# Kernel tuning notes

Measured on AMD Instinct MI355X. Metric: run time of the kernel, lower is better.

Reference implementation:

```python
import jax, jax.numpy as jnp
import numpy as np

B, CI, CO, H, W, E, R, K = 32, 128, 256, 64, 64, 8, 16, 3


def setup_inputs() -> dict:
    key = jax.random.key(0)
    ks = jax.random.split(key, 12)
    def n(k, shape, scale):
        return jax.random.normal(k, shape, dtype=jnp.float32) * scale
    return {
        "x": n(ks[0], (B, CI, H, W), 1.0),
        "experts": n(ks[1], (E, CO, CI, K, K), 0.1),
        # routing SE: C -> C/R -> C -> E (1x1 convs == dense on pooled vec)
        "rw1": n(ks[2], (CI // R, CI), 0.05), "rb1": jnp.zeros((CI // R,), jnp.float32),
        "rw2": n(ks[3], (CI, CI // R), 0.05), "rb2": jnp.zeros((CI,), jnp.float32),
        "rw3": n(ks[4], (E, CI), 0.05),      "rb3": jnp.zeros((E,), jnp.float32),
        # channel attention SE on output: CO -> CO/R -> CO
        "aw1": n(ks[5], (CO // R, CO), 0.05), "ab1": jnp.zeros((CO // R,), jnp.float32),
        "aw2": n(ks[6], (CO, CO // R), 0.05), "ab2": jnp.zeros((CO,), jnp.float32),
    }


def reference(x, experts, rw1, rb1, rw2, rb2, rw3, rb3, aw1, ab1, aw2, ab2):
    # --- routing: SE-style gate -> softmax over experts ---
    pooled = x.mean(axis=(2, 3))                       # [B, CI]
    h = jax.nn.relu(pooled @ rw1.T + rb1)              # [B, CI/R]
    s = jax.nn.sigmoid(h @ rw2.T + rb2)                # [B, CI]
    rweights = jax.nn.softmax(s @ rw3.T + rb3, axis=1) # [B, E]
    # --- per-sample expert kernel combination ---
    w = jnp.einsum('be,eoihw->boihw', rweights, experts)  # [B, CO, CI, K, K]
    # --- per-sample conv (== grouped conv with groups=B) via vmap ---
    def conv1(xi, wi):
        # xi: [CI,H,W], wi: [CO,CI,K,K]
        return jax.lax.conv_general_dilated(
            xi[None], wi, window_strides=(1, 1), padding=[(1, 1), (1, 1)],
            dimension_numbers=('NCHW', 'OIHW', 'NCHW'))[0]
    out = jax.vmap(conv1)(x, w)                        # [B, CO, H, W]
    # --- channel attention on output ---
    p = out.mean(axis=(2, 3))                          # [B, CO]
    ca = jax.nn.sigmoid(jax.nn.relu(p @ aw1.T + ab1) @ aw2.T + ab2)
    return out * ca[:, :, None, None]
```

## Files before the change

### kernel.cpp

```cpp
#include <hip/hip_runtime.h>
#include <hip/hip_bf16.h>


#define BB 32
#define CI_ 128
#define CO_ 256
#define HW_ 4096
#define KK 1152

typedef unsigned short u16;
typedef __attribute__((ext_vector_type(8))) __bf16 bf16x8;
typedef __attribute__((ext_vector_type(4))) float floatx4;

typedef const __attribute__((address_space(1))) void* gptr_t;
typedef __attribute__((address_space(3))) void* sptr_t;

__device__ __forceinline__ void gload_lds16(const void* g, void* s) {
  __builtin_amdgcn_global_load_lds((gptr_t)g, (sptr_t)s, 16, 0, 0);
}

__global__ __launch_bounds__(256) void k_stats2(const float* __restrict__ x,
                                                float* __restrict__ Sr,
                                                float* __restrict__ pooled,
                                                unsigned* __restrict__ zp) {
  int blk = blockIdx.x;
  int tid = threadIdx.x;
  if (blk == 0 && tid < 64) zp[tid] = 0u;
  int b = blk >> 7, ci = blk & 127;
  const float4* xp = (const float4*)(x + ((size_t)(b * CI_ + ci) << 12));
  float T = 0.f, r0 = 0.f, r63 = 0.f, c0 = 0.f, c63 = 0.f;
  __shared__ float corn[4];
  __shared__ float wsum[4][5];
#pragma unroll
  for (int j = 0; j < 4; j++) {
    int idx = j * 256 + tid;
    float4 v = xp[idx];
    float rs = v.x + v.y + v.z + v.w;
    T += rs;
    int x16 = idx & 15;
    if (idx < 16)    r0  += rs;
    if (idx >= 1008) r63 += rs;
    if (x16 == 0)  c0  += v.x;
    if (x16 == 15) c63 += v.w;
    if (idx == 0)    corn[0] = v.x;
    if (idx == 15)   corn[1] = v.w;
    if (idx == 1008) corn[2] = v.x;
    if (idx == 1023) corn[3] = v.w;
  }
  for (int off = 32; off; off >>= 1) {
    T   += __shfl_down(T, off);
    r0  += __shfl_down(r0, off);
    r63 += __shfl_down(r63, off);
    c0  += __shfl_down(c0, off);
    c63 += __shfl_down(c63, off);
  }
  int w = tid >> 6, lane = tid & 63;
  if (lane == 0) { wsum[w][0]=T; wsum[w][1]=r0; wsum[w][2]=r63; wsum[w][3]=c0; wsum[w][4]=c63; }
  __syncthreads();
  if (tid == 0) {
    T   = wsum[0][0]+wsum[1][0]+wsum[2][0]+wsum[3][0];
    r0  = wsum[0][1]+wsum[1][1]+wsum[2][1]+wsum[3][1];
    r63 = wsum[0][2]+wsum[1][2]+wsum[2][2]+wsum[3][2];
    c0  = wsum[0][3]+wsum[1][3]+wsum[2][3]+wsum[3][3];
    c63 = wsum[0][4]+wsum[1][4]+wsum[2][4]+wsum[3][4];
    pooled[b * CI_ + ci] = T * (1.0f / 4096.0f);
#pragma unroll
    for (int ky = 0; ky < 3; ky++) {
#pragma unroll
      for (int kx = 0; kx < 3; kx++) {
        int dy = ky - 1, dx = kx - 1;
        float s = T;
        if (dy == -1) s -= r63;
        if (dy ==  1) s -= r0;
        if (dx == -1) s -= c63;
        if (dx ==  1) s -= c0;
        if (dy != 0 && dx != 0) s += corn[(dy == -1 ? 2 : 0) + (dx == -1 ? 1 : 0)];
        Sr[(b * 9 + ky * 3 + kx) * CI_ + ci] = s * (1.0f / 4096.0f);
      }
    }
  }
}

__global__ __launch_bounds__(256) void k_xform(const float* __restrict__ x,
                                               u16* __restrict__ xt) {
  int blk = blockIdx.x;
  int b = blk >> 6, y = blk & 63;
  __shared__ u16 ts[64][132];
  int tid = threadIdx.x;
  const float* xb = x + ((size_t)b << 19) + (y << 6);
#pragma unroll
  for (int it = 0; it < 8; it++) {
    int idx = it * 256 + tid;
    int ci = idx >> 4, x4 = idx & 15;
    float4 v = *(const float4*)(xb + (size_t)ci * 4096 + x4 * 4);
    __hip_bfloat16 h0 = __float2bfloat16(v.x), h1 = __float2bfloat16(v.y);
    __hip_bfloat16 h2 = __float2bfloat16(v.z), h3 = __float2bfloat16(v.w);
    int xx = x4 << 2;
    ts[xx + 0][ci] = *(const u16*)&h0;
    ts[xx + 1][ci] = *(const u16*)&h1;
    ts[xx + 2][ci] = *(const u16*)&h2;
    ts[xx + 3][ci] = *(const u16*)&h3;
  }
  __syncthreads();
  uint2* ot = (uint2*)(xt + ((size_t)b * HW_ + y * 64) * CI_);
#pragma unroll
  for (int it = 0; it < 8; it++) {
    int o = it * 256 + tid;
    int pix = o >> 5, c4 = o & 31;
    ot[o] = *(const uint2*)&ts[pix][c4 * 4];
  }
}

__global__ __launch_bounds__(128) void k_route2(const float* __restrict__ pooled,
    const float* __restrict__ rw1, const float* __restrict__ rb1,
    const float* __restrict__ rw2, const float* __restrict__ rb2,
    const float* __restrict__ rw3, const float* __restrict__ rb3,
    float* __restrict__ r) {
  int b = blockIdx.x, tid = threadIdx.x;
  int o = tid >> 4, l = tid & 15;
  __shared__ float ps[128], hs[8], ss[128], lg[8];
  ps[tid] = pooled[b * 128 + tid];
  __syncthreads();
  {
    float a = 0.f;
#pragma unroll
    for (int j = 0; j < 8; j++) a += ps[l * 8 + j] * rw1[o * 128 + l * 8 + j];
    a += __shfl_xor(a, 1); a += __shfl_xor(a, 2);
    a += __shfl_xor(a, 4); a += __shfl_xor(a, 8);
    if (l == 0) hs[o] = fmaxf(a + rb1[o], 0.f);
  }
  __syncthreads();
  {
    float a = rb2[tid];
#pragma unroll
    for (int j = 0; j < 8; j++) a += hs[j] * rw2[tid * 8 + j];
    ss[tid] = 1.f / (1.f + expf(-a));
  }
  __syncthreads();
  {
    float a = 0.f;
#pragma unroll
    for (int j = 0; j < 8; j++) a += ss[l * 8 + j] * rw3[o * 128 + l * 8 + j];
    a += __shfl_xor(a, 1); a += __shfl_xor(a, 2);
    a += __shfl_xor(a, 4); a += __shfl_xor(a, 8);
    if (l == 0) lg[o] = a + rb3[o];
  }
  __syncthreads();
  if (tid == 0) {
    float m = lg[0];
    for (int e = 1; e < 8; e++) m = fmaxf(m, lg[e]);
    float s = 0.f, ex[8];
    for (int e = 0; e < 8; e++) { ex[e] = expf(lg[e] - m); s += ex[e]; }
    for (int e = 0; e < 8; e++) r[b * 8 + e] = ex[e] / s;
  }
}

__global__ __launch_bounds__(256) void k_combine2(const float* __restrict__ experts,
                                                  const float* __restrict__ r,
                                                  const float* __restrict__ Sr,
                                                  __hip_bfloat16* __restrict__ wr,
                                                  float* __restrict__ p) {
  int co = blockIdx.x & 255, g = blockIdx.x >> 8;
  int tid = threadIdx.x;
  __shared__ float els[8][1152];
  __shared__ float rsh[32][8];
  __shared__ float pw[4];
#pragma unroll
  for (int it = 0; it < 9; it++) {
    int f = it * 256 + tid;
    int e = f / 288, q = f - e * 288;
    float4 ev = *(const float4*)(experts + (size_t)e * 294912 + (size_t)co * 1152 + q * 4);
    *(float4*)&els[e][q * 4] = ev;
  }
  rsh[tid >> 3][tid & 7] = r[tid];
  __syncthreads();
  int s = tid >> 7, ci = tid & 127;
  for (int bb = 0; bb < 4; bb++) {
    int b = g * 8 + bb * 2 + s;
    float rv[8];
#pragma unroll
    for (int e = 0; e < 8; e++) rv[e] = rsh[b][e];
    float pacc = 0.f;
    __hip_bfloat16* wrow = wr + (size_t)(b * 256 + co) * KK;
    const float* sb = Sr + b * KK;
#pragma unroll
    for (int k = 0; k < 9; k++) {
      float v = 0.f;
#pragma unroll
      for (int e = 0; e < 8; e++) v += rv[e] * els[e][ci * 9 + k];
      wrow[k * 128 + ci] = __float2bfloat16(v);
      pacc += v * sb[k * 128 + ci];
    }
    for (int off = 32; off; off >>= 1) pacc += __shfl_down(pacc, off);
    if ((tid & 63) == 0) pw[tid >> 6] = pacc;
    __syncthreads();
    if (ci == 0) p[b * 256 + co] = pw[s * 2] + pw[s * 2 + 1];
    __syncthreads();
  }
}

__global__ __launch_bounds__(256) void k_catt2(const float* __restrict__ p,
    const float* __restrict__ aw1, const float* __restrict__ ab1,
    const float* __restrict__ aw2, const float* __restrict__ ab2,
    float* __restrict__ ca) {
  int b = blockIdx.x, tid = threadIdx.x;
  int o = tid >> 4, l = tid & 15;
  __shared__ float ps[256], ts[16];
  ps[tid] = p[b * 256 + tid];
  __syncthreads();
  {
    float a = 0.f;
#pragma unroll
    for (int j = 0; j < 16; j++) a += ps[l * 16 + j] * aw1[o * 256 + l * 16 + j];
    a += __shfl_xor(a, 1); a += __shfl_xor(a, 2);
    a += __shfl_xor(a, 4); a += __shfl_xor(a, 8);
    if (l == 0) ts[o] = fmaxf(a + ab1[o], 0.f);
  }
  __syncthreads();
  float a = ab2[tid];
#pragma unroll
  for (int j = 0; j < 16; j++) a += ts[j] * aw2[tid * 16 + j];
  ca[b * 256 + tid] = 1.f / (1.f + expf(-a));
}

__global__ __launch_bounds__(256) void k_conv(const u16* __restrict__ xt,
                                              const u16* __restrict__ wr,
                                              const float* __restrict__ ca,
                                              const u16* __restrict__ zp,
                                              float* __restrict__ out) {
  int id = blockIdx.x;
  int b = (id & 7) | (((id >> 9) & 3) << 3);
  int rem = (id >> 3) & 63;
  int coT = rem >> 5, rp = rem & 31;
  int y0 = rp * 2;
  int coBase = coT * 128;
  int tid = threadIdx.x;
  int w = tid >> 6, lane = tid & 63;
  int wm = w & 1, wn = w >> 1;
  int quad = lane >> 4, l15 = lane & 15;
  int cl8 = lane & 7, lr = lane >> 3;

  __shared__ __align__(16) u16 As[128 * 64];
  __shared__ __align__(16) u16 Bs[128 * 64];

  const u16* aP[4];
  int dstO[4], chB[4], ylocB[4], xlocB[4];
#pragma unroll
  for (int ri = 0; ri < 4; ri++) {
    int rr = ri * 32 + w * 8 + lr;
    int c = cl8 ^ (rr & 7);
    aP[ri] = wr + (size_t)(b * 256 + coBase + rr) * KK + c * 8;
    dstO[ri] = rr * 64 + cl8 * 8;
    chB[ri] = c;
    ylocB[ri] = rr >> 6;
    xlocB[ri] = rr & 63;
  }

  int aOff[4][2], bOff[4][2];
#pragma unroll
  for (int i = 0; i < 4; i++) {
    int m = wm * 64 + i * 16 + l15;
    int n = wn * 64 + i * 16 + l15;
#pragma unroll
    for (int h = 0; h < 2; h++) {
      aOff[i][h] = m * 64 + ((((h << 2) | quad) ^ (m & 7)) << 3);
      bOff[i][h] = n * 64 + ((((h << 2) | quad) ^ (n & 7)) << 3);
    }
  }

  floatx4 acc[4][4];
#pragma unroll
  for (int i = 0; i < 4; i++)
#pragma unroll
    for (int j = 0; j < 4; j++) acc[i][j] = floatx4{0.f, 0.f, 0.f, 0.f};

  for (int kidx = 0; kidx < 9; kidx++) {
    int ky = kidx / 3, kx = kidx - ky * 3;
    const u16* bP[4];
    int bStep[4];
#pragma unroll
    for (int ri = 0; ri < 4; ri++) {
      int ys = y0 + ylocB[ri] + ky - 1;
      int xs = xlocB[ri] + kx - 1;
      bool valid = ((unsigned)ys < 64u) && ((unsigned)xs < 64u);
      bP[ri] = valid ? (xt + ((size_t)(b * HW_ + ys * 64 + xs) << 7) + chB[ri] * 8)
                     : (zp + chB[ri] * 8);
      bStep[ri] = valid ? 64 : 0;
    }
#pragma unroll
    for (int cib = 0; cib < 2; cib++) {
      __syncthreads();
#pragma unroll
      for (int ri = 0; ri < 4; ri++)
        gload_lds16(aP[ri] + kidx * 128 + cib * 64, &As[dstO[ri]]);
#pragma unroll
      for (int ri = 0; ri < 4; ri++)
        gload_lds16(bP[ri] + cib * bStep[ri], &Bs[dstO[ri]]);
      __syncthreads();
#pragma unroll
      for (int h = 0; h < 2; h++) {
        bf16x8 af[4], bfv[4];
#pragma unroll
        for (int i = 0; i < 4; i++) af[i] = *(const bf16x8*)&As[aOff[i][h]];
#pragma unroll
        for (int j = 0; j < 4; j++) bfv[j] = *(const bf16x8*)&Bs[bOff[j][h]];
#pragma unroll
        for (int i = 0; i < 4; i++)
#pragma unroll
          for (int j = 0; j < 4; j++)
            acc[i][j] = __builtin_amdgcn_mfma_f32_16x16x32_bf16(af[i], bfv[j], acc[i][j], 0, 0, 0);
      }
    }
  }

  float cav[4][4];
#pragma unroll
  for (int i = 0; i < 4; i++)
#pragma unroll
    for (int ri = 0; ri < 4; ri++)
      cav[i][ri] = ca[b * 256 + coBase + wm * 64 + i * 16 + quad * 4 + ri];
#pragma unroll
  for (int i = 0; i < 4; i++) {
#pragma unroll
    for (int j = 0; j < 4; j++) {
      int n = wn * 64 + j * 16 + l15;
      int yy = y0 + (n >> 6), xx = n & 63;
#pragma unroll
      for (int ri = 0; ri < 4; ri++) {
        int co = coBase + wm * 64 + i * 16 + quad * 4 + ri;
        out[((size_t)(b * 256 + co) << 12) + (yy << 6) + xx] = acc[i][j][ri] * cav[i][ri];
      }
    }
  }
}

extern "C" void kernel_launch(void* const* d_in, const int* in_sizes, int n_in,
                              void* d_out, int out_size, void* d_ws, size_t ws_size,
                              hipStream_t stream) {
  const float* x       = (const float*)d_in[0];
  const float* experts = (const float*)d_in[1];
  const float* rw1 = (const float*)d_in[2];
  const float* rb1 = (const float*)d_in[3];
  const float* rw2 = (const float*)d_in[4];
  const float* rb2 = (const float*)d_in[5];
  const float* rw3 = (const float*)d_in[6];
  const float* rb3 = (const float*)d_in[7];
  const float* aw1 = (const float*)d_in[8];
  const float* ab1 = (const float*)d_in[9];
  const float* aw2 = (const float*)d_in[10];
  const float* ab2 = (const float*)d_in[11];

  char* ws = (char*)d_ws;
  u16*   xt     = (u16*)(ws + 0);
  __hip_bfloat16* wr = (__hip_bfloat16*)(ws + 33554432);
  float* Sr     = (float*)(ws + 52428800);
  float* pooled = (float*)(ws + 52576256);
  float* r      = (float*)(ws + 52592640);
  float* p      = (float*)(ws + 52593664);
  float* ca     = (float*)(ws + 52626432);
  u16*   zp     = (u16*)(ws + 52659200);

  k_stats2<<<4096, 256, 0, stream>>>(x, Sr, pooled, (unsigned*)zp);
  k_xform<<<2048, 256, 0, stream>>>(x, xt);
  k_route2<<<32, 128, 0, stream>>>(pooled, rw1, rb1, rw2, rb2, rw3, rb3, r);
  k_combine2<<<1024, 256, 0, stream>>>(experts, r, Sr, wr, p);
  k_catt2<<<32, 256, 0, stream>>>(p, aw1, ab1, aw2, ab2, ca);
  k_conv<<<2048, 256, 0, stream>>>(xt, (const u16*)wr, ca, zp, (float*)d_out);
}
```

Before: 311.4 us.

## Enlarge conv tile to 256x256 with double-buffered LDS prefetch

The conv kernel now uses 512-thread blocks, each computing all 256 output channels for four image rows (a 256x256 output tile), instead of 128x128 tiles. LDS is double-buffered, so the next K-slice's global-to-LDS loads are issued before the current slice's MFMAs, and the loop needs one barrier per step instead of two. This is meant to reuse each input tile across all output channels, cut redundant loads, and hide load latency. In exchange it uses 128 accumulator registers per thread and 128KB of LDS per block, and launches only 512 blocks, which may limit occupancy.

After: 321.1 us. 3.1% more time.

```diff
diff --git a/kernel.cpp b/kernel.cpp
--- a/kernel.cpp
+++ b/kernel.cpp
@@ -223,112 +223,128 @@
   ca[b * 256 + tid] = 1.f / (1.f + expf(-a));
 }
 
-__global__ __launch_bounds__(256) void k_conv(const u16* __restrict__ xt,
-                                              const u16* __restrict__ wr,
-                                              const float* __restrict__ ca,
-                                              const u16* __restrict__ zp,
-                                              float* __restrict__ out) {
+__global__ __launch_bounds__(512, 2) void k_conv2p(const u16* __restrict__ xt,
+                                                   const u16* __restrict__ wr,
+                                                   const float* __restrict__ ca,
+                                                   const u16* __restrict__ zp,
+                                                   float* __restrict__ out) {
+  __shared__ __align__(16) u16 As[2 * 16384];
+  __shared__ __align__(16) u16 Bs[2 * 16384];
+
   int id = blockIdx.x;
-  int b = (id & 7) | (((id >> 9) & 3) << 3);
-  int rem = (id >> 3) & 63;
-  int coT = rem >> 5, rp = rem & 31;
-  int y0 = rp * 2;
-  int coBase = coT * 128;
+  int swz = (id & 7) * 64 + (id >> 3);
+  int b = swz >> 4, posT = swz & 15;
+  int y0 = posT * 4;
+
   int tid = threadIdx.x;
   int w = tid >> 6, lane = tid & 63;
-  int wm = w & 1, wn = w >> 1;
+  int wm = w >> 2, wn = w & 3;
   int quad = lane >> 4, l15 = lane & 15;
-  int cl8 = lane & 7, lr = lane >> 3;
-
-  __shared__ __align__(16) u16 As[128 * 64];
-  __shared__ __align__(16) u16 Bs[128 * 64];
-
-  const u16* aP[4];
-  int dstO[4], chB[4], ylocB[4], xlocB[4];
-#pragma unroll
-  for (int ri = 0; ri < 4; ri++) {
-    int rr = ri * 32 + w * 8 + lr;
-    int c = cl8 ^ (rr & 7);
-    aP[ri] = wr + (size_t)(b * 256 + coBase + rr) * KK + c * 8;
-    dstO[ri] = rr * 64 + cl8 * 8;
-    chB[ri] = c;
-    ylocB[ri] = rr >> 6;
-    xlocB[ri] = rr & 63;
-  }
-
-  int aOff[4][2], bOff[4][2];
-#pragma unroll
-  for (int i = 0; i < 4; i++) {
-    int m = wm * 64 + i * 16 + l15;
-    int n = wn * 64 + i * 16 + l15;
-#pragma unroll
-    for (int h = 0; h < 2; h++) {
-      aOff[i][h] = m * 64 + ((((h << 2) | quad) ^ (m & 7)) << 3);
-      bOff[i][h] = n * 64 + ((((h << 2) | quad) ^ (n & 7)) << 3);
-    }
-  }
-
-  floatx4 acc[4][4];
-#pragma unroll
-  for (int i = 0; i < 4; i++)
+
+  int rowT = tid >> 3;
+  int srcChunk = (tid & 7) ^ (rowT & 7);
+  int ldsOff = tid * 8;
+  const u16* aBase = wr + (size_t)b * (256 * KK) + (size_t)rowT * KK + srcChunk * 8;
+  const u16* xtB = xt + ((size_t)b << 19);
+  const u16* zpS = zp + srcChunk * 8;
+
+  int aRow[4], bRow[2];
+#pragma unroll
+  for (int i2 = 0; i2 < 4; i2++) aRow[i2] = (wm * 128 + i2 * 16 + l15) << 6;
+#pragma unroll
+  for (int j2 = 0; j2 < 2; j2++) bRow[j2] = (wn * 64 + j2 * 16 + l15) << 6;
+  int chA0 = (quad ^ (l15 & 7)) << 3;
+  int chA1 = ((4 ^ quad) ^ (l15 & 7)) << 3;
+
+  floatx4 acc[8][4];
+#pragma unroll
+  for (int i = 0; i < 8; i++)
 #pragma unroll
     for (int j = 0; j < 4; j++) acc[i][j] = floatx4{0.f, 0.f, 0.f, 0.f};
 
-  for (int kidx = 0; kidx < 9; kidx++) {
-    int ky = kidx / 3, kx = kidx - ky * 3;
-    const u16* bP[4];
-    int bStep[4];
-#pragma unroll
-    for (int ri = 0; ri < 4; ri++) {
-      int ys = y0 + ylocB[ri] + ky - 1;
-      int xs = xlocB[ri] + kx - 1;
-      bool valid = ((unsigned)ys < 64u) && ((unsigned)xs < 64u);
-      bP[ri] = valid ? (xt + ((size_t)(b * HW_ + ys * 64 + xs) << 7) + chB[ri] * 8)
-                     : (zp + chB[ri] * 8);
-      bStep[ri] = valid ? 64 : 0;
-    }
-#pragma unroll
-    for (int cib = 0; cib < 2; cib++) {
-      __syncthreads();
-#pragma unroll
-      for (int ri = 0; ri < 4; ri++)
-        gload_lds16(aP[ri] + kidx * 128 + cib * 64, &As[dstO[ri]]);
-#pragma unroll
-      for (int ri = 0; ri < 4; ri++)
-        gload_lds16(bP[ri] + cib * bStep[ri], &Bs[dstO[ri]]);
-      __syncthreads();
-#pragma unroll
-      for (int h = 0; h < 2; h++) {
-        bf16x8 af[4], bfv[4];
-#pragma unroll
-        for (int i = 0; i < 4; i++) af[i] = *(const bf16x8*)&As[aOff[i][h]];
-#pragma unroll
-        for (int j = 0; j < 4; j++) bfv[j] = *(const bf16x8*)&Bs[bOff[j][h]];
-#pragma unroll
-        for (int i = 0; i < 4; i++)
-#pragma unroll
-          for (int j = 0; j < 4; j++)
-            acc[i][j] = __builtin_amdgcn_mfma_f32_16x16x32_bf16(af[i], bfv[j], acc[i][j], 0, 0, 0);
+  auto SA = [&](int q, int ktS, int bufL) {
+    gload_lds16(aBase + (size_t)q * (64 * KK) + ktS * 64,
+                &As[(bufL << 14) + (q << 12) + ldsOff]);
+  };
+  auto SB = [&](int q, int ktS, int bufL) {
+    int kidx = ktS >> 1;
+    int ky = (kidx * 11) >> 5;
+    int kx = kidx - ky * 3;
+    int ys = y0 + q + ky - 1;
+    int xs = rowT + kx - 1;
+    const u16* src = (((unsigned)ys < 64u) && ((unsigned)xs < 64u))
+        ? xtB + (((size_t)(ys * 64 + xs)) << 7) + ((ktS & 1) << 6) + srcChunk * 8
+        : zpS;
+    gload_lds16(src, &Bs[(bufL << 14) + (q << 12) + ldsOff]);
+  };
+
+  SA(0, 0, 0); SA(1, 0, 0); SA(2, 0, 0); SA(3, 0, 0);
+  SB(0, 0, 0); SB(1, 0, 0); SB(2, 0, 0); SB(3, 0, 0);
+  __syncthreads();
+
+  for (int t = 0; t < 18; t++) {
+    int cur = t & 1;
+    if (t < 17) {
+      int nxt = cur ^ 1;
+      SA(0, t + 1, nxt); SA(1, t + 1, nxt); SA(2, t + 1, nxt); SA(3, t + 1, nxt);
+      SB(0, t + 1, nxt); SB(1, t + 1, nxt); SB(2, t + 1, nxt); SB(3, t + 1, nxt);
+    }
+    int cb = cur << 14;
+    bf16x8 af[4][2], bv0[2][2], bv1[2][2];
+#pragma unroll
+    for (int i2 = 0; i2 < 4; i2++) {
+      af[i2][0] = *(const bf16x8*)&As[cb + aRow[i2] + chA0];
+      af[i2][1] = *(const bf16x8*)&As[cb + aRow[i2] + chA1];
+    }
+#pragma unroll
+    for (int j2 = 0; j2 < 2; j2++) {
+      bv0[j2][0] = *(const bf16x8*)&Bs[cb + bRow[j2] + chA0];
+      bv0[j2][1] = *(const bf16x8*)&Bs[cb + bRow[j2] + chA1];
+      bv1[j2][0] = *(const bf16x8*)&Bs[cb + bRow[j2] + (1 << 11) + chA0];
+      bv1[j2][1] = *(const bf16x8*)&Bs[cb + bRow[j2] + (1 << 11) + chA1];
+    }
+#pragma unroll
+    for (int i2 = 0; i2 < 4; i2++)
+#pragma unroll
+      for (int j2 = 0; j2 < 2; j2++) {
+        acc[i2][j2] = __builtin_amdgcn_mfma_f32_16x16x32_bf16(af[i2][0], bv0[j2][0], acc[i2][j2], 0, 0, 0);
+        acc[i2][j2] = __builtin_amdgcn_mfma_f32_16x16x32_bf16(af[i2][1], bv0[j2][1], acc[i2][j2], 0, 0, 0);
+        acc[i2][2 + j2] = __builtin_amdgcn_mfma_f32_16x16x32_bf16(af[i2][0], bv1[j2][0], acc[i2][2 + j2], 0, 0, 0);
+        acc[i2][2 + j2] = __builtin_amdgcn_mfma_f32_16x16x32_bf16(af[i2][1], bv1[j2][1], acc[i2][2 + j2], 0, 0, 0);
       }
-    }
-  }
-
-  float cav[4][4];
-#pragma unroll
-  for (int i = 0; i < 4; i++)
-#pragma unroll
-    for (int ri = 0; ri < 4; ri++)
-      cav[i][ri] = ca[b * 256 + coBase + wm * 64 + i * 16 + quad * 4 + ri];
-#pragma unroll
-  for (int i = 0; i < 4; i++) {
-#pragma unroll
-    for (int j = 0; j < 4; j++) {
-      int n = wn * 64 + j * 16 + l15;
-      int yy = y0 + (n >> 6), xx = n & 63;
+#pragma unroll
+    for (int i2 = 0; i2 < 4; i2++) {
+      af[i2][0] = *(const bf16x8*)&As[cb + aRow[i2] + (1 << 12) + chA0];
+      af[i2][1] = *(const bf16x8*)&As[cb + aRow[i2] + (1 << 12) + chA1];
+    }
+#pragma unroll
+    for (int i2 = 0; i2 < 4; i2++)
+#pragma unroll
+      for (int j2 = 0; j2 < 2; j2++) {
+        acc[4 + i2][j2] = __builtin_amdgcn_mfma_f32_16x16x32_bf16(af[i2][0], bv0[j2][0], acc[4 + i2][j2], 0, 0, 0);
+        acc[4 + i2][j2] = __builtin_amdgcn_mfma_f32_16x16x32_bf16(af[i2][1], bv0[j2][1], acc[4 + i2][j2], 0, 0, 0);
+        acc[4 + i2][2 + j2] = __builtin_amdgcn_mfma_f32_16x16x32_bf16(af[i2][0], bv1[j2][0], acc[4 + i2][2 + j2], 0, 0, 0);
+        acc[4 + i2][2 + j2] = __builtin_amdgcn_mfma_f32_16x16x32_bf16(af[i2][1], bv1[j2][1], acc[4 + i2][2 + j2], 0, 0, 0);
+      }
+    asm volatile("s_waitcnt vmcnt(0)" ::: "memory");
+    __syncthreads();
+  }
+
+  const float* caB = ca + b * 256 + wm * 128 + quad * 4;
+  float cav[8][4];
+#pragma unroll
+  for (int mf = 0; mf < 8; mf++)
+#pragma unroll
+    for (int ri = 0; ri < 4; ri++) cav[mf][ri] = caB[mf * 16 + ri];
+  float* outB = out + ((size_t)b << 20) + ((size_t)(wm * 128 + quad * 4) << 12)
+              + posT * 256 + wn * 64 + l15;
+#pragma unroll
+  for (int mf = 0; mf < 8; mf++) {
+#pragma unroll
+    for (int nf = 0; nf < 4; nf++) {
 #pragma unroll
       for (int ri = 0; ri < 4; ri++) {
-        int co = coBase + wm * 64 + i * 16 + quad * 4 + ri;
-        out[((size_t)(b * 256 + co) << 12) + (yy << 6) + xx] = acc[i][j][ri] * cav[i][ri];
+        outB[(((size_t)(mf * 16 + ri)) << 12) + nf * 16] = acc[mf][nf][ri] * cav[mf][ri];
       }
     }
   }
@@ -365,5 +381,5 @@
   k_route2<<<32, 128, 0, stream>>>(pooled, rw1, rb1, rw2, rb2, rw3, rb3, r);
   k_combine2<<<1024, 256, 0, stream>>>(experts, r, Sr, wr, p);
   k_catt2<<<32, 256, 0, stream>>>(p, aw1, ab1, aw2, ab2, ca);
-  k_conv<<<2048, 256, 0, stream>>>(xt, (const u16*)wr, ca, zp, (float*)d_out);
-}
+  k_conv2p<<<512, 512, 0, stream>>>(xt, (const u16*)wr, ca, zp, (float*)d_out);
+}
```

## Fuse input statistics into transpose kernel and merge stats finalize with routing

Applied to the files above, without the earlier changes.

Drops the separate stats pass over x, which re-read the whole 64MB input. The transpose/bf16 conversion kernel now also computes per-row sums, column edge sums and corners, accumulating them with atomics into scratch that aliases the weight buffer, and is preceded by memsets. A small finalize kernel builds the pooled means and the shifted-window sums and then runs the routing MLP. It trades one full-input read and one launch for float atomics, which make accumulation order nondeterministic, and for two extra memsets.

Result: no change. 313.9 us (+0.8%).

```diff
diff --git a/kernel.cpp b/kernel.cpp
--- a/kernel.cpp
+++ b/kernel.cpp
@@ -19,70 +19,14 @@
   __builtin_amdgcn_global_load_lds((gptr_t)g, (sptr_t)s, 16, 0, 0);
 }
 
-__global__ __launch_bounds__(256) void k_stats2(const float* __restrict__ x,
-                                                float* __restrict__ Sr,
-                                                float* __restrict__ pooled,
-                                                unsigned* __restrict__ zp) {
-  int blk = blockIdx.x;
-  int tid = threadIdx.x;
-  if (blk == 0 && tid < 64) zp[tid] = 0u;
-  int b = blk >> 7, ci = blk & 127;
-  const float4* xp = (const float4*)(x + ((size_t)(b * CI_ + ci) << 12));
-  float T = 0.f, r0 = 0.f, r63 = 0.f, c0 = 0.f, c63 = 0.f;
-  __shared__ float corn[4];
-  __shared__ float wsum[4][5];
-#pragma unroll
-  for (int j = 0; j < 4; j++) {
-    int idx = j * 256 + tid;
-    float4 v = xp[idx];
-    float rs = v.x + v.y + v.z + v.w;
-    T += rs;
-    int x16 = idx & 15;
-    if (idx < 16)    r0  += rs;
-    if (idx >= 1008) r63 += rs;
-    if (x16 == 0)  c0  += v.x;
-    if (x16 == 15) c63 += v.w;
-    if (idx == 0)    corn[0] = v.x;
-    if (idx == 15)   corn[1] = v.w;
-    if (idx == 1008) corn[2] = v.x;
-    if (idx == 1023) corn[3] = v.w;
-  }
-  for (int off = 32; off; off >>= 1) {
-    T   += __shfl_down(T, off);
-    r0  += __shfl_down(r0, off);
-    r63 += __shfl_down(r63, off);
-    c0  += __shfl_down(c0, off);
-    c63 += __shfl_down(c63, off);
-  }
-  int w = tid >> 6, lane = tid & 63;
-  if (lane == 0) { wsum[w][0]=T; wsum[w][1]=r0; wsum[w][2]=r63; wsum[w][3]=c0; wsum[w][4]=c63; }
-  __syncthreads();
-  if (tid == 0) {
-    T   = wsum[0][0]+wsum[1][0]+wsum[2][0]+wsum[3][0];
-    r0  = wsum[0][1]+wsum[1][1]+wsum[2][1]+wsum[3][1];
-    r63 = wsum[0][2]+wsum[1][2]+wsum[2][2]+wsum[3][2];
-    c0  = wsum[0][3]+wsum[1][3]+wsum[2][3]+wsum[3][3];
-    c63 = wsum[0][4]+wsum[1][4]+wsum[2][4]+wsum[3][4];
-    pooled[b * CI_ + ci] = T * (1.0f / 4096.0f);
-#pragma unroll
-    for (int ky = 0; ky < 3; ky++) {
-#pragma unroll
-      for (int kx = 0; kx < 3; kx++) {
-        int dy = ky - 1, dx = kx - 1;
-        float s = T;
-        if (dy == -1) s -= r63;
-        if (dy ==  1) s -= r0;
-        if (dx == -1) s -= c63;
-        if (dx ==  1) s -= c0;
-        if (dy != 0 && dx != 0) s += corn[(dy == -1 ? 2 : 0) + (dx == -1 ? 1 : 0)];
-        Sr[(b * 9 + ky * 3 + kx) * CI_ + ci] = s * (1.0f / 4096.0f);
-      }
-    }
-  }
-}
-
-__global__ __launch_bounds__(256) void k_xform(const float* __restrict__ x,
-                                               u16* __restrict__ xt) {
+__global__ __launch_bounds__(256) void k_prep(const float* __restrict__ x,
+                                              u16* __restrict__ xt,
+                                              float* __restrict__ Tb,
+                                              float* __restrict__ C0a,
+                                              float* __restrict__ C63a,
+                                              float* __restrict__ R0a,
+                                              float* __restrict__ R63a,
+                                              float* __restrict__ CNa) {
   int blk = blockIdx.x;
   int b = blk >> 6, y = blk & 63;
   __shared__ u16 ts[64][132];
@@ -93,6 +37,18 @@
     int idx = it * 256 + tid;
     int ci = idx >> 4, x4 = idx & 15;
     float4 v = *(const float4*)(xb + (size_t)ci * 4096 + x4 * 4);
+    float rs = v.x + v.y + v.z + v.w;
+    rs += __shfl_xor(rs, 1); rs += __shfl_xor(rs, 2);
+    rs += __shfl_xor(rs, 4); rs += __shfl_xor(rs, 8);
+    float ce = __shfl(v.w, 15, 16);
+    if (x4 == 0) {
+      int o = b * 128 + ci;
+      atomicAdd(&Tb[o], rs);
+      atomicAdd(&C0a[o], v.x);
+      atomicAdd(&C63a[o], ce);
+      if (y == 0)  { R0a[o]  = rs; CNa[o * 4 + 0] = v.x; CNa[o * 4 + 1] = ce; }
+      if (y == 63) { R63a[o] = rs; CNa[o * 4 + 2] = v.x; CNa[o * 4 + 3] = ce; }
+    }
     __hip_bfloat16 h0 = __float2bfloat16(v.x), h1 = __float2bfloat16(v.y);
     __hip_bfloat16 h2 = __float2bfloat16(v.z), h3 = __float2bfloat16(v.w);
     int xx = x4 << 2;
@@ -111,23 +67,48 @@
   }
 }
 
-__global__ __launch_bounds__(128) void k_route2(const float* __restrict__ pooled,
+__global__ __launch_bounds__(128) void k_statsfin(const float* __restrict__ Tb,
+    const float* __restrict__ C0a, const float* __restrict__ C63a,
+    const float* __restrict__ R0a, const float* __restrict__ R63a,
+    const float* __restrict__ CNa,
+    float* __restrict__ Sr,
     const float* __restrict__ rw1, const float* __restrict__ rb1,
     const float* __restrict__ rw2, const float* __restrict__ rb2,
     const float* __restrict__ rw3, const float* __restrict__ rb3,
     float* __restrict__ r) {
   int b = blockIdx.x, tid = threadIdx.x;
-  int o = tid >> 4, l = tid & 15;
+  int o = b * 128 + tid;
+  float T   = Tb[o];
+  float r0  = R0a[o],  r63 = R63a[o];
+  float c0  = C0a[o],  c63 = C63a[o];
+  float cn[4];
+  cn[0] = CNa[o * 4 + 0]; cn[1] = CNa[o * 4 + 1];
+  cn[2] = CNa[o * 4 + 2]; cn[3] = CNa[o * 4 + 3];
   __shared__ float ps[128], hs[8], ss[128], lg[8];
-  ps[tid] = pooled[b * 128 + tid];
-  __syncthreads();
+  ps[tid] = T * (1.0f / 4096.0f);
+#pragma unroll
+  for (int ky = 0; ky < 3; ky++) {
+#pragma unroll
+    for (int kx = 0; kx < 3; kx++) {
+      int dy = ky - 1, dx = kx - 1;
+      float s = T;
+      if (dy == -1) s -= r63;
+      if (dy ==  1) s -= r0;
+      if (dx == -1) s -= c63;
+      if (dx ==  1) s -= c0;
+      if (dy != 0 && dx != 0) s += cn[(dy == -1 ? 2 : 0) + (dx == -1 ? 1 : 0)];
+      Sr[(b * 9 + ky * 3 + kx) * CI_ + tid] = s * (1.0f / 4096.0f);
+    }
+  }
+  __syncthreads();
+  int oo = tid >> 4, l = tid & 15;
   {
     float a = 0.f;
 #pragma unroll
-    for (int j = 0; j < 8; j++) a += ps[l * 8 + j] * rw1[o * 128 + l * 8 + j];
+    for (int j = 0; j < 8; j++) a += ps[l * 8 + j] * rw1[oo * 128 + l * 8 + j];
     a += __shfl_xor(a, 1); a += __shfl_xor(a, 2);
     a += __shfl_xor(a, 4); a += __shfl_xor(a, 8);
-    if (l == 0) hs[o] = fmaxf(a + rb1[o], 0.f);
+    if (l == 0) hs[oo] = fmaxf(a + rb1[oo], 0.f);
   }
   __syncthreads();
   {
@@ -140,10 +121,10 @@
   {
     float a = 0.f;
 #pragma unroll
-    for (int j = 0; j < 8; j++) a += ss[l * 8 + j] * rw3[o * 128 + l * 8 + j];
+    for (int j = 0; j < 8; j++) a += ss[l * 8 + j] * rw3[oo * 128 + l * 8 + j];
     a += __shfl_xor(a, 1); a += __shfl_xor(a, 2);
     a += __shfl_xor(a, 4); a += __shfl_xor(a, 8);
-    if (l == 0) lg[o] = a + rb3[o];
+    if (l == 0) lg[oo] = a + rb3[oo];
   }
   __syncthreads();
   if (tid == 0) {
@@ -354,15 +335,24 @@
   u16*   xt     = (u16*)(ws + 0);
   __hip_bfloat16* wr = (__hip_bfloat16*)(ws + 33554432);
   float* Sr     = (float*)(ws + 52428800);
-  float* pooled = (float*)(ws + 52576256);
   float* r      = (float*)(ws + 52592640);
   float* p      = (float*)(ws + 52593664);
   float* ca     = (float*)(ws + 52626432);
   u16*   zp     = (u16*)(ws + 52659200);
 
-  k_stats2<<<4096, 256, 0, stream>>>(x, Sr, pooled, (unsigned*)zp);
-  k_xform<<<2048, 256, 0, stream>>>(x, xt);
-  k_route2<<<32, 128, 0, stream>>>(pooled, rw1, rb1, rw2, rb2, rw3, rb3, r);
+  float* Tb   = (float*)(ws + 33554432);
+  float* C0a  = Tb + 4096;
+  float* C63a = Tb + 8192;
+  float* R0a  = Tb + 12288;
+  float* R63a = Tb + 16384;
+  float* CNa  = Tb + 20480;
+
+  hipMemsetAsync(Tb, 0, 3 * 16384, stream);
+  hipMemsetAsync(zp, 0, 256, stream);
+
+  k_prep<<<2048, 256, 0, stream>>>(x, xt, Tb, C0a, C63a, R0a, R63a, CNa);
+  k_statsfin<<<32, 128, 0, stream>>>(Tb, C0a, C63a, R0a, R63a, CNa, Sr,
+                                     rw1, rb1, rw2, rb2, rw3, rb3, r);
   k_combine2<<<1024, 256, 0, stream>>>(experts, r, Sr, wr, p);
   k_catt2<<<32, 256, 0, stream>>>(p, aw1, ab1, aw2, ab2, ca);
   k_conv<<<2048, 256, 0, stream>>>(xt, (const u16*)wr, ca, zp, (float*)d_out);
```
